# Kernel tuning notes

Hardware: AMD Instinct MI355X
Metric: run time of the kernel (lower is better)

Reference implementation:

```python
import jax, jax.numpy as jnp
import numpy as np

SEQ = 512      # sentence length n
WD, TD = 100, 28
IN = WD + TD   # 128, lstm input size == hidden size
H = IN         # 128
D = 2 * H      # 256, biLSTM output per token
MLP_IN = 2 * D # 512
HID = MLP_IN   # 512, MLP hidden (hidden_size=mlpInputSize)
V, T = 50000, 50


def setup_inputs() -> dict:
    key = jax.random.key(0)
    keys = iter(jax.random.split(key, 64))
    def nrm(shape, s=0.1):
        return jax.random.normal(next(keys), shape, jnp.float32) * s
    inp = {}
    inp["word_ids"] = jax.random.randint(next(keys), (SEQ,), 0, V)
    inp["tag_ids"] = jax.random.randint(next(keys), (SEQ,), 0, T)
    inp["word_emb_table"] = nrm((V, WD))
    inp["tag_emb_table"] = nrm((T, TD))
    # initHiddenCellState: randn, layout [layer*2+dir, hidden] (batch=1 squeezed)
    inp["h0"] = nrm((4, H), 1.0)
    inp["c0"] = nrm((4, H), 1.0)
    # 2-layer biLSTM params; layer0 input IN, layer1 input 2*H
    for l, insz in ((0, IN), (1, 2 * H)):
        for d in ("f", "b"):
            inp[f"Wih_l{l}{d}"] = nrm((4 * H, insz))
            inp[f"Whh_l{l}{d}"] = nrm((4 * H, H))
            inp[f"bih_l{l}{d}"] = nrm((4 * H,))
            inp[f"bhh_l{l}{d}"] = nrm((4 * H,))
    # MLP: Linear(MLP_IN, HID) -> tanh -> Linear(HID, 1)
    inp["W1"] = nrm((HID, MLP_IN))
    inp["b1"] = nrm((HID,))
    inp["W2"] = nrm((1, HID))
    inp["b2"] = nrm((1,))
    return inp


def _run_dir(x, Wih, Whh, bih, bhh, h0, c0, rev):
    # x: [S, in]; returns hidden states [S, H]
    xs = x[::-1] if rev else x
    pre = xs @ Wih.T + bih + bhh  # precompute input contribution [S, 4H]
    def step(carry, p):
        h, c = carry
        g = p + h @ Whh.T
        i, f, gg, o = jnp.split(g, 4)
        i, f, o = jax.nn.sigmoid(i), jax.nn.sigmoid(f), jax.nn.sigmoid(o)
        c = f * c + i * jnp.tanh(gg)
        h = o * jnp.tanh(c)
        return (h, c), h
    _, hs = jax.lax.scan(step, (h0, c0), pre)
    return hs[::-1] if rev else hs


def reference(word_ids, tag_ids, word_emb_table, tag_emb_table, h0, c0,
              Wih_l0f, Whh_l0f, bih_l0f, bhh_l0f,
              Wih_l0b, Whh_l0b, bih_l0b, bhh_l0b,
              Wih_l1f, Whh_l1f, bih_l1f, bhh_l1f,
              Wih_l1b, Whh_l1b, bih_l1b, bhh_l1b,
              W1, b1, W2, b2):
    # embed + concat: [S, IN]
    x = jnp.concatenate([word_emb_table[word_ids], tag_emb_table[tag_ids]], axis=1)
    layers = [((Wih_l0f, Whh_l0f, bih_l0f, bhh_l0f), (Wih_l0b, Whh_l0b, bih_l0b, bhh_l0b)),
              ((Wih_l1f, Whh_l1f, bih_l1f, bhh_l1f), (Wih_l1b, Whh_l1b, bih_l1b, bhh_l1b))]
    h = x
    for l, (pf, pb) in enumerate(layers):
        hf = _run_dir(h, *pf, h0[2 * l], c0[2 * l], False)
        hb = _run_dir(h, *pb, h0[2 * l + 1], c0[2 * l + 1], True)
        h = jnp.concatenate([hf, hb], axis=1)  # [S, 2H]
    # batched pairwise MLP: score(i,j) = W2 @ tanh(W1 @ [h_i; h_j] + b1) + b2
    W1a, W1b = W1[:, :D], W1[:, D:]
    A = h @ W1a.T  # [S, HID]
    B = h @ W1b.T  # [S, HID]
    hmid = jnp.tanh(A[:, None, :] + B[None, :, :] + b1)  # [S, S, HID]
    scores = jnp.einsum('nmh,h->nm', hmid, W2[0]) + b2[0]
    # diagonal never written in the original (permutations exclude i==i)
    scores = scores * (1.0 - jnp.eye(SEQ, dtype=scores.dtype))
    # column normalization by column sums
    scores = scores / scores.sum(axis=0, keepdims=True)
    # nn.Softmax() on 2D -> dim=1
    return jax.nn.softmax(scores, axis=1)
```

## Files before the change

kernel.cpp:

```cpp
#include <hip/hip_runtime.h>

#define LOG2E 1.4426950408889634f
#define TWO_LOG2E 2.8853900817779268f

#if __has_builtin(__builtin_amdgcn_exp2f)
__device__ __forceinline__ float fexp2(float x){ return __builtin_amdgcn_exp2f(x); }
#else
__device__ __forceinline__ float fexp2(float x){ return exp2f(x); }
#endif
#if __has_builtin(__builtin_amdgcn_rcpf)
__device__ __forceinline__ float frcp(float x){ return __builtin_amdgcn_rcpf(x); }
#else
__device__ __forceinline__ float frcp(float x){ return 1.0f/(x); }
#endif

template<int CTRL>
__device__ __forceinline__ float dpp_f(float x) {
    return __int_as_float(__builtin_amdgcn_update_dpp(0, __float_as_int(x), CTRL, 0xF, 0xF, true));
}
#define DPP_XOR1  0xB1
#define DPP_XOR2  0x4E
#define DPP_BC0   0x00
#define DPP_BC1   0x55
#define DPP_BC2   0xAA
#define DPP_BC3   0xFF

__global__ __launch_bounds__(256) void gemm_l0(
    const int* __restrict__ wid, const int* __restrict__ tgi,
    const float* __restrict__ wemb, const float* __restrict__ temb,
    const float* __restrict__ Wa, const float* __restrict__ Wb,
    const float* __restrict__ b1a, const float* __restrict__ b1b,
    const float* __restrict__ b2a, const float* __restrict__ b2b,
    float* __restrict__ Ca, float* __restrict__ Cb,
    float* __restrict__ csum)
{
    int tid = threadIdx.x;
    if (blockIdx.x == 0 && blockIdx.y == 0 && blockIdx.z == 0) {
        csum[tid] = 0.f; csum[tid + 256] = 0.f;
    }
    int z = blockIdx.z;
    const float* W   = z ? Wb  : Wa;
    const float* bb1 = z ? b1b : b1a;
    const float* bb2 = z ? b2b : b2a;
    float* C = z ? Cb : Ca;

    __shared__ float Xs[64*33];
    __shared__ float Ws[64*33];
    int tx = tid & 15, ty = tid >> 4;
    int n0 = blockIdx.y*64, r0 = blockIdx.x*64;
    float acc[4][4] = {};

    for (int k0 = 0; k0 < 128; k0 += 32) {
        #pragma unroll
        for (int i = 0; i < 2; ++i) {
            int idx = tid + 256*i;
            int row = idx >> 3, c4 = idx & 7;
            int k = k0 + c4*4;
            int rg = n0 + row;
            float4 vx = (k < 100) ? *(const float4*)(wemb + wid[rg]*100 + k)
                                  : *(const float4*)(temb + tgi[rg]*28 + (k-100));
            float4 vw = *(const float4*)(W + (r0+row)*128 + k0 + c4*4);
            Xs[row*33 + c4*4+0]=vx.x; Xs[row*33 + c4*4+1]=vx.y; Xs[row*33 + c4*4+2]=vx.z; Xs[row*33 + c4*4+3]=vx.w;
            Ws[row*33 + c4*4+0]=vw.x; Ws[row*33 + c4*4+1]=vw.y; Ws[row*33 + c4*4+2]=vw.z; Ws[row*33 + c4*4+3]=vw.w;
        }
        __syncthreads();
        #pragma unroll 8
        for (int kk = 0; kk < 32; ++kk) {
            float a[4], b[4];
            #pragma unroll
            for (int i = 0; i < 4; ++i) a[i] = Xs[(4*ty+i)*33 + kk];
            #pragma unroll
            for (int j = 0; j < 4; ++j) b[j] = Ws[(4*tx+j)*33 + kk];
            #pragma unroll
            for (int i = 0; i < 4; ++i)
                #pragma unroll
                for (int j = 0; j < 4; ++j)
                    acc[i][j] = fmaf(a[i], b[j], acc[i][j]);
        }
        __syncthreads();
    }
    #pragma unroll
    for (int i = 0; i < 4; ++i)
        #pragma unroll
        for (int j = 0; j < 4; ++j) {
            int r = r0 + 4*tx + j;
            C[(n0 + 4*ty + i)*512 + r] = acc[i][j] + bb1[r] + bb2[r];
        }
}

__global__ __launch_bounds__(256) void gemm2(
    const float* __restrict__ X, int ldx,
    const float* __restrict__ Wa, const float* __restrict__ Wb, int ldw, int woffb,
    const float* __restrict__ b1a, const float* __restrict__ b1b,
    const float* __restrict__ b2a, const float* __restrict__ b2b,
    float* __restrict__ Ca, float* __restrict__ Cb,
    int K, float scale)
{
    int z = blockIdx.z;
    const float* W  = z ? Wb  : Wa;
    const float* bb1 = z ? b1b : b1a;
    const float* bb2 = z ? b2b : b2a;
    float* C = z ? Cb : Ca;
    int woff = z ? woffb : 0;

    __shared__ float Xs[64*33];
    __shared__ float Ws[64*33];
    int tid = threadIdx.x;
    int tx = tid & 15, ty = tid >> 4;
    int n0 = blockIdx.y*64, r0 = blockIdx.x*64;
    float acc[4][4] = {};

    for (int k0 = 0; k0 < K; k0 += 32) {
        #pragma unroll
        for (int i = 0; i < 2; ++i) {
            int idx = tid + 256*i;
            int row = idx >> 3, c4 = idx & 7;
            float4 vx = *(const float4*)(X + (n0+row)*ldx + k0 + c4*4);
            float4 vw = *(const float4*)(W + (r0+row)*ldw + woff + k0 + c4*4);
            Xs[row*33 + c4*4+0]=vx.x; Xs[row*33 + c4*4+1]=vx.y; Xs[row*33 + c4*4+2]=vx.z; Xs[row*33 + c4*4+3]=vx.w;
            Ws[row*33 + c4*4+0]=vw.x; Ws[row*33 + c4*4+1]=vw.y; Ws[row*33 + c4*4+2]=vw.z; Ws[row*33 + c4*4+3]=vw.w;
        }
        __syncthreads();
        #pragma unroll 8
        for (int kk = 0; kk < 32; ++kk) {
            float a[4], b[4];
            #pragma unroll
            for (int i = 0; i < 4; ++i) a[i] = Xs[(4*ty+i)*33 + kk];
            #pragma unroll
            for (int j = 0; j < 4; ++j) b[j] = Ws[(4*tx+j)*33 + kk];
            #pragma unroll
            for (int i = 0; i < 4; ++i)
                #pragma unroll
                for (int j = 0; j < 4; ++j)
                    acc[i][j] = fmaf(a[i], b[j], acc[i][j]);
        }
        __syncthreads();
    }
    #pragma unroll
    for (int i = 0; i < 4; ++i)
        #pragma unroll
        for (int j = 0; j < 4; ++j) {
            int r = r0 + 4*tx + j;
            float v = acc[i][j];
            if (bb1) v += bb1[r];
            if (bb2) v += bb2[r];
            C[(n0 + 4*ty + i)*512 + r] = v*scale;
        }
}

__global__ __launch_bounds__(512, 2) void lstm_kernel(
    const float* __restrict__ preF, const float* __restrict__ preB,
    const float* __restrict__ WhhF, const float* __restrict__ WhhB,
    const float* __restrict__ h0, const float* __restrict__ c0,
    float* __restrict__ hout, int layer)
{
    const int dir = blockIdx.x;
    const int tid = threadIdx.x;
    const int sub = tid & 3;
    const int j   = tid >> 2;
    const int q   = sub;
    const float* Whh  = dir ? WhhB : WhhF;
    const float* preD = dir ? preB : preF;

    int cidx[8];
    #pragma unroll
    for (int k = 0; k < 8; ++k) cidx[k] = (sub << 3) + ((k + 2*sub) & 7);

    float w[4][32];
    #pragma unroll
    for (int r = 0; r < 4; ++r) {
        const float* wr = Whh + ((r << 7) + j)*128;
        #pragma unroll
        for (int k = 0; k < 8; ++k) {
            float4 v = *(const float4*)(wr + 4*cidx[k]);
            w[r][4*k+0]=v.x; w[r][4*k+1]=v.y; w[r][4*k+2]=v.z; w[r][4*k+3]=v.w;
        }
    }

    __shared__ __align__(16) float hbuf[2][128];

    const float* h0d = h0 + (2*layer + dir)*128;
    const float* c0d = c0 + (2*layer + dir)*128;
    float c = c0d[j];
    if (tid < 128) hbuf[0][tid] = h0d[tid];

    const float sc = (q == 2) ? -TWO_LOG2E : -LOG2E;
    const int prow = (q << 7) + j;
    const int t0 = dir ? 511 : 0;
    const int dt = dir ? -1 : 1;

    float pcur = preD[t0*512 + prow];
    __syncthreads();

    #pragma unroll 2
    for (int s = 0; s < 512; ++s) {
        const int t  = t0 + dt*s;
        const int tn = (s < 511) ? (t + dt) : t;
        float pnext = preD[tn*512 + prow];

        const int p = s & 1;
        const float4* h4 = (const float4*)hbuf[p];
        float4 hv[8];
        #pragma unroll
        for (int k = 0; k < 8; ++k) hv[k] = h4[cidx[k]];

        float acc[4] = {0.f, 0.f, 0.f, 0.f};
        #pragma unroll
        for (int k = 0; k < 8; ++k) {
            #pragma unroll
            for (int r = 0; r < 4; ++r) {
                acc[r] = fmaf(hv[k].x, w[r][4*k+0], acc[r]);
                acc[r] = fmaf(hv[k].y, w[r][4*k+1], acc[r]);
                acc[r] = fmaf(hv[k].z, w[r][4*k+2], acc[r]);
                acc[r] = fmaf(hv[k].w, w[r][4*k+3], acc[r]);
            }
        }

        #pragma unroll
        for (int r = 0; r < 4; ++r) {
            acc[r] += dpp_f<DPP_XOR1>(acc[r]);
            acc[r] += dpp_f<DPP_XOR2>(acc[r]);
        }

        float a01 = (q & 1) ? acc[1] : acc[0];
        float a23 = (q & 1) ? acc[3] : acc[2];
        float xg  = (((q & 2) ? a23 : a01) + pcur) * sc;
        float sv  = frcp(1.f + fexp2(xg));

        float vi = dpp_f<DPP_BC0>(sv);
        float vf = dpp_f<DPP_BC1>(sv);
        float vg = dpp_f<DPP_BC2>(sv);
        float vo = dpp_f<DPP_BC3>(sv);

        float tg = fmaf(2.f, vg, -1.f);
        c = fmaf(vf, c, vi*tg);
        float th = fmaf(-2.f, frcp(1.f + fexp2(TWO_LOG2E*c)), 1.f);
        float h  = vo * th;

        if (sub == 1) hbuf[p ^ 1][j] = h;
        if (sub == 2) hout[t*256 + dir*128 + j] = h;
        __syncthreads();
        pcur = pnext;
    }
}

__global__ __launch_bounds__(256) void score_kernel(
    const float* __restrict__ Ap, const float* __restrict__ Bp,
    const float* __restrict__ W2, const float* __restrict__ b2p,
    float* __restrict__ S, float* __restrict__ csum)
{
    __shared__ __align__(16) float As[32*132];
    __shared__ __align__(16) float Bs[16*132];
    __shared__ __align__(16) float W2s[128];
    __shared__ float ps[16][17];
    int tid = threadIdx.x;
    int tx = tid & 15, ty = tid >> 4;
    int m0 = blockIdx.x*16, n0 = blockIdx.y*32;
    float acc0 = 0.f, acc1 = 0.f;

    for (int hc = 0; hc < 512; hc += 128) {
        #pragma unroll
        for (int i = 0; i < 4; ++i) {
            int idx = tid + 256*i;
            int row = idx >> 5, c4 = idx & 31;
            *(float4*)&As[row*132 + c4*4] = *(const float4*)(Ap + (n0+row)*512 + hc + c4*4);
        }
        #pragma unroll
        for (int i = 0; i < 2; ++i) {
            int idx = tid + 256*i;
            int row = idx >> 5, c4 = idx & 31;
            *(float4*)&Bs[row*132 + c4*4] = *(const float4*)(Bp + (m0+row)*512 + hc + c4*4);
        }
        if (tid < 128) W2s[tid] = W2[hc + tid];
        __syncthreads();

        #pragma unroll 4
        for (int h4 = 0; h4 < 32; ++h4) {
            float4 a0 = *(const float4*)&As[ty*132 + 4*h4];
            float4 a1 = *(const float4*)&As[(ty+16)*132 + 4*h4];
            float4 bv = *(const float4*)&Bs[tx*132 + 4*h4];
            float4 w4 = *(const float4*)&W2s[4*h4];
            float aa0[4] = {a0.x,a0.y,a0.z,a0.w};
            float aa1[4] = {a1.x,a1.y,a1.z,a1.w};
            float bb[4]  = {bv.x,bv.y,bv.z,bv.w};
            float ww[4]  = {w4.x,w4.y,w4.z,w4.w};
            #pragma unroll
            for (int qi = 0; qi < 4; ++qi) {
                float r0v = frcp(1.f + fexp2(aa0[qi] + bb[qi]));
                float r1v = frcp(1.f + fexp2(aa1[qi] + bb[qi]));
                acc0 = fmaf(ww[qi], fmaf(-2.f, r0v, 1.f), acc0);
                acc1 = fmaf(ww[qi], fmaf(-2.f, r1v, 1.f), acc1);
            }
        }
        __syncthreads();
    }

    float b2s = b2p[0];
    int gm  = m0 + tx;
    int gn0 = n0 + ty;
    int gn1 = n0 + 16 + ty;
    float v0 = acc0 + b2s; if (gn0 == gm) v0 = 0.f;
    float v1 = acc1 + b2s; if (gn1 == gm) v1 = 0.f;
    S[gn0*512 + gm] = v0;
    S[gn1*512 + gm] = v1;

    ps[ty][tx] = v0 + v1;
    __syncthreads();
    if (tid < 16) {
        float s = 0.f;
        #pragma unroll
        for (int k = 0; k < 16; ++k) s += ps[k][tid];
        atomicAdd(&csum[m0 + tid], s);
    }
}

__global__ __launch_bounds__(256) void softmax_kernel(const float* __restrict__ S,
                                                      const float* __restrict__ csum,
                                                      float* __restrict__ out)
{
    int n = blockIdx.x, tid = threadIdx.x;
    float v0 = S[n*512 + tid]       / csum[tid];
    float v1 = S[n*512 + tid + 256] / csum[tid + 256];

    __shared__ float rbuf[4], rbuf2[4];
    int wid = tid >> 6;

    float mx = fmaxf(v0, v1);
    #pragma unroll
    for (int off = 32; off; off >>= 1) mx = fmaxf(mx, __shfl_xor(mx, off, 64));
    if ((tid & 63) == 0) rbuf[wid] = mx;
    __syncthreads();
    mx = fmaxf(fmaxf(rbuf[0], rbuf[1]), fmaxf(rbuf[2], rbuf[3]));

    float e0 = fexp2((v0 - mx)*LOG2E);
    float e1 = fexp2((v1 - mx)*LOG2E);
    float sm = e0 + e1;
    #pragma unroll
    for (int off = 32; off; off >>= 1) sm += __shfl_xor(sm, off, 64);
    if ((tid & 63) == 0) rbuf2[wid] = sm;
    __syncthreads();
    sm = (rbuf2[0] + rbuf2[1]) + (rbuf2[2] + rbuf2[3]);

    float inv = 1.0f / sm;
    out[n*512 + tid]       = e0*inv;
    out[n*512 + tid + 256] = e1*inv;
}

extern "C" void kernel_launch(void* const* d_in, const int* in_sizes, int n_in,
                              void* d_out, int out_size, void* d_ws, size_t ws_size,
                              hipStream_t stream)
{
    const int*   wid  = (const int*)d_in[0];
    const int*   tgi  = (const int*)d_in[1];
    const float* wemb = (const float*)d_in[2];
    const float* temb = (const float*)d_in[3];
    const float* h0   = (const float*)d_in[4];
    const float* c0   = (const float*)d_in[5];
    const float* Wih0f=(const float*)d_in[6],  *Whh0f=(const float*)d_in[7],  *bih0f=(const float*)d_in[8],  *bhh0f=(const float*)d_in[9];
    const float* Wih0b=(const float*)d_in[10], *Whh0b=(const float*)d_in[11], *bih0b=(const float*)d_in[12], *bhh0b=(const float*)d_in[13];
    const float* Wih1f=(const float*)d_in[14], *Whh1f=(const float*)d_in[15], *bih1f=(const float*)d_in[16], *bhh1f=(const float*)d_in[17];
    const float* Wih1b=(const float*)d_in[18], *Whh1b=(const float*)d_in[19], *bih1b=(const float*)d_in[20], *bhh1b=(const float*)d_in[21];
    const float* W1   = (const float*)d_in[22];
    const float* b1   = (const float*)d_in[23];
    const float* W2   = (const float*)d_in[24];
    const float* b2   = (const float*)d_in[25];

    float* ws    = (float*)d_ws;
    float* h0cat = ws;
    float* h1cat = ws + 131072;
    float* pA    = ws + 262144;
    float* pB    = ws + 524288;
    float* S     = ws;
    float* csum  = ws + 786432;
    float* out   = (float*)d_out;

    gemm_l0<<<dim3(8,8,2), 256, 0, stream>>>(wid, tgi, wemb, temb,
                                             Wih0f, Wih0b, bih0f, bih0b, bhh0f, bhh0b,
                                             pA, pB, csum);
    lstm_kernel<<<2, 512, 0, stream>>>(pA, pB, Whh0f, Whh0b, h0, c0, h0cat, 0);

    gemm2<<<dim3(8,8,2), 256, 0, stream>>>(h0cat, 256, Wih1f, Wih1b, 256, 0,
                                           bih1f, bih1b, bhh1f, bhh1b,
                                           pA, pB, 256, 1.0f);
    lstm_kernel<<<2, 512, 0, stream>>>(pA, pB, Whh1f, Whh1b, h0, c0, h1cat, 1);

    gemm2<<<dim3(8,8,2), 256, 0, stream>>>(h1cat, 256, W1, W1, 512, 256,
                                           b1, nullptr, nullptr, nullptr,
                                           pA, pB, 256, TWO_LOG2E);

    score_kernel<<<dim3(32,16), 256, 0, stream>>>(pA, pB, W2, b2, S, csum);
    softmax_kernel<<<512, 256, 0, stream>>>(S, csum, out);
}
```

Before: 760.7 us.

## Compute LSTM recurrent matvec with fp16 MFMA instead of scalar FMAs

The per-step Whh·h product is moved from per-thread fp32 FMAs with DPP reductions onto 16x16x32 fp16 MFMA instructions. Weights are held as fp16 fragments in registers and the hidden state is stored in shared memory as fp16. Thread-to-cell mapping is rearranged so the accumulator lanes line up with the gate broadcast. The barrier is replaced with an inline waitcnt+s_barrier, and the index arithmetic with pointer increments. This trades precision (fp16 weights and h) for a shorter serial critical path per timestep. It also adds a wasteful pattern: each accumulator has a 4x-redundant layout in which a matrix-vector product is padded into 16 columns.

Result: faster. 639.9 us (median of 2 runs) (-15.9%).

```diff
diff --git a/kernel.cpp b/kernel.cpp
--- a/kernel.cpp
+++ b/kernel.cpp
@@ -18,12 +18,14 @@
 __device__ __forceinline__ float dpp_f(float x) {
     return __int_as_float(__builtin_amdgcn_update_dpp(0, __float_as_int(x), CTRL, 0xF, 0xF, true));
 }
-#define DPP_XOR1  0xB1
-#define DPP_XOR2  0x4E
 #define DPP_BC0   0x00
 #define DPP_BC1   0x55
 #define DPP_BC2   0xAA
 #define DPP_BC3   0xFF
+
+typedef unsigned int u32;
+typedef _Float16 f16x8 __attribute__((ext_vector_type(8)));
+typedef float    f32x4 __attribute__((ext_vector_type(4)));
 
 __global__ __launch_bounds__(256) void gemm_l0(
     const int* __restrict__ wid, const int* __restrict__ tgi,
@@ -156,75 +158,86 @@
 {
     const int dir = blockIdx.x;
     const int tid = threadIdx.x;
-    const int sub = tid & 3;
-    const int j   = tid >> 2;
-    const int q   = sub;
+    const int l   = tid & 63;
+    const int w   = tid >> 6;
+    const int j   = l & 15;
+    const int kb  = l >> 4;
+    const int q   = j & 3;
+    const int rsel= j >> 2;
+    const int cell= 16*w + 4*kb + rsel;
     const float* Whh  = dir ? WhhB : WhhF;
     const float* preD = dir ? preB : preF;
 
-    int cidx[8];
+    f16x8 afr[4][4];
     #pragma unroll
-    for (int k = 0; k < 8; ++k) cidx[k] = (sub << 3) + ((k + 2*sub) & 7);
-
-    float w[4][32];
-    #pragma unroll
-    for (int r = 0; r < 4; ++r) {
-        const float* wr = Whh + ((r << 7) + j)*128;
-        #pragma unroll
-        for (int k = 0; k < 8; ++k) {
-            float4 v = *(const float4*)(wr + 4*cidx[k]);
-            w[r][4*k+0]=v.x; w[r][4*k+1]=v.y; w[r][4*k+2]=v.z; w[r][4*k+3]=v.w;
-        }
-    }
-
-    __shared__ __align__(16) float hbuf[2][128];
+    for (int g = 0; g < 4; ++g) {
+        const float* wr = Whh + ((g << 7) + 16*w + j)*128 + (kb << 3);
+        #pragma unroll
+        for (int kc = 0; kc < 4; ++kc) {
+            float4 u = *(const float4*)(wr + (kc << 5));
+            float4 v = *(const float4*)(wr + (kc << 5) + 4);
+            f16x8 a;
+            a[0]=(_Float16)u.x; a[1]=(_Float16)u.y; a[2]=(_Float16)u.z; a[3]=(_Float16)u.w;
+            a[4]=(_Float16)v.x; a[5]=(_Float16)v.y; a[6]=(_Float16)v.z; a[7]=(_Float16)v.w;
+            afr[g][kc] = a;
+        }
+    }
+
+    __shared__ __align__(16) _Float16 hbuf[2][128];
 
     const float* h0d = h0 + (2*layer + dir)*128;
     const float* c0d = c0 + (2*layer + dir)*128;
-    float c = c0d[j];
-    if (tid < 128) hbuf[0][tid] = h0d[tid];
+    float c = c0d[cell];
+    if (tid < 128) hbuf[0][tid] = (_Float16)h0d[tid];
 
     const float sc = (q == 2) ? -TWO_LOG2E : -LOG2E;
-    const int prow = (q << 7) + j;
+    const int prow = (q << 7) + cell;
     const int t0 = dir ? 511 : 0;
     const int dt = dir ? -1 : 1;
-
-    float pcur = preD[t0*512 + prow];
+    const int pstep = dt*512;
+    const int hstep = dt*256;
+
+    const float* pptr = preD + t0*512 + prow;
+    float*       hptr = hout + t0*256 + dir*128 + cell;
+
+    const f32x4 zacc = {0.f, 0.f, 0.f, 0.f};
+
+    float pcur = *pptr;
     __syncthreads();
 
     #pragma unroll 2
     for (int s = 0; s < 512; ++s) {
-        const int t  = t0 + dt*s;
-        const int tn = (s < 511) ? (t + dt) : t;
-        float pnext = preD[tn*512 + prow];
+        pptr += pstep;
+        float pnext = *pptr;
 
         const int p = s & 1;
-        const float4* h4 = (const float4*)hbuf[p];
-        float4 hv[8];
-        #pragma unroll
-        for (int k = 0; k < 8; ++k) hv[k] = h4[cidx[k]];
-
-        float acc[4] = {0.f, 0.f, 0.f, 0.f};
-        #pragma unroll
-        for (int k = 0; k < 8; ++k) {
-            #pragma unroll
-            for (int r = 0; r < 4; ++r) {
-                acc[r] = fmaf(hv[k].x, w[r][4*k+0], acc[r]);
-                acc[r] = fmaf(hv[k].y, w[r][4*k+1], acc[r]);
-                acc[r] = fmaf(hv[k].z, w[r][4*k+2], acc[r]);
-                acc[r] = fmaf(hv[k].w, w[r][4*k+3], acc[r]);
-            }
-        }
-
-        #pragma unroll
-        for (int r = 0; r < 4; ++r) {
-            acc[r] += dpp_f<DPP_XOR1>(acc[r]);
-            acc[r] += dpp_f<DPP_XOR2>(acc[r]);
-        }
-
-        float a01 = (q & 1) ? acc[1] : acc[0];
-        float a23 = (q & 1) ? acc[3] : acc[2];
-        float xg  = (((q & 2) ? a23 : a01) + pcur) * sc;
+        const uint4* h4 = (const uint4*)hbuf[p];
+        f16x8 bf[4];
+        #pragma unroll
+        for (int kc = 0; kc < 4; ++kc)
+            bf[kc] = __builtin_bit_cast(f16x8, h4[4*kc + kb]);
+
+        f32x4 ac0 = __builtin_amdgcn_mfma_f32_16x16x32_f16(afr[0][0], bf[0], zacc, 0,0,0);
+        f32x4 ac1 = __builtin_amdgcn_mfma_f32_16x16x32_f16(afr[1][0], bf[0], zacc, 0,0,0);
+        f32x4 ac2 = __builtin_amdgcn_mfma_f32_16x16x32_f16(afr[2][0], bf[0], zacc, 0,0,0);
+        f32x4 ac3 = __builtin_amdgcn_mfma_f32_16x16x32_f16(afr[3][0], bf[0], zacc, 0,0,0);
+        #pragma unroll
+        for (int kc = 1; kc < 4; ++kc) {
+            ac0 = __builtin_amdgcn_mfma_f32_16x16x32_f16(afr[0][kc], bf[kc], ac0, 0,0,0);
+            ac1 = __builtin_amdgcn_mfma_f32_16x16x32_f16(afr[1][kc], bf[kc], ac1, 0,0,0);
+            ac2 = __builtin_amdgcn_mfma_f32_16x16x32_f16(afr[2][kc], bf[kc], ac2, 0,0,0);
+            ac3 = __builtin_amdgcn_mfma_f32_16x16x32_f16(afr[3][kc], bf[kc], ac3, 0,0,0);
+        }
+
+        float x0 = (rsel & 2) ? ((rsel & 1) ? ac0[3] : ac0[2]) : ((rsel & 1) ? ac0[1] : ac0[0]);
+        float x1 = (rsel & 2) ? ((rsel & 1) ? ac1[3] : ac1[2]) : ((rsel & 1) ? ac1[1] : ac1[0]);
+        float x2 = (rsel & 2) ? ((rsel & 1) ? ac2[3] : ac2[2]) : ((rsel & 1) ? ac2[1] : ac2[0]);
+        float x3 = (rsel & 2) ? ((rsel & 1) ? ac3[3] : ac3[2]) : ((rsel & 1) ? ac3[1] : ac3[0]);
+        float v01 = (q & 1) ? x1 : x0;
+        float v23 = (q & 1) ? x3 : x2;
+        float V   = (q & 2) ? v23 : v01;
+
+        float xg  = (V + pcur) * sc;
         float sv  = frcp(1.f + fexp2(xg));
 
         float vi = dpp_f<DPP_BC0>(sv);
@@ -237,9 +250,10 @@
         float th = fmaf(-2.f, frcp(1.f + fexp2(TWO_LOG2E*c)), 1.f);
         float h  = vo * th;
 
-        if (sub == 1) hbuf[p ^ 1][j] = h;
-        if (sub == 2) hout[t*256 + dir*128 + j] = h;
-        __syncthreads();
+        if (q == 1) hbuf[p ^ 1][cell] = (_Float16)h;
+        if (q == 2) *hptr = h;
+        hptr += hstep;
+        asm volatile("s_waitcnt lgkmcnt(0)\n\ts_barrier" ::: "memory");
         pcur = pnext;
     }
 }
```
